# Performance work log

Measured on AMD Instinct MI355X. Metric: run time of the kernel, lower is better.

The kernel has to match this reference:

```python
import jax, jax.numpy as jnp
import numpy as np

N = 65536      # total voxels (lidar + image tokens)
D = 256        # d_model
H = 8          # nhead
DFF = 2048     # dim_feedforward
SS = 128       # set_size
SN = 512       # set_num (SN * SS == N, each partition is a permutation of all voxels)
NSHIFT = 2


def setup_inputs() -> dict:
    key = jax.random.key(0)
    ks = jax.random.split(key, 10)
    src = jax.random.normal(ks[0], (N, D), jnp.float32)
    pos_embed = jax.random.normal(ks[1], (NSHIFT, N, D), jnp.float32) * 0.02
    # each (shift, set_id) partition covers every voxel exactly once
    inds = jnp.stack([
        jnp.stack([
            jax.random.permutation(jax.random.fold_in(ks[2], s * 2 + p), N).reshape(SN, SS)
            for p in range(2)
        ])
        for s in range(NSHIFT)
    ]).astype(jnp.int32)                      # (NSHIFT, 2, SN, SS)
    masks = jax.random.uniform(ks[3], (NSHIFT, 2, SN, SS)) < 0.1
    masks = masks.at[..., 0].set(False)       # keep at least one key per set
    init = lambda k, shape: jax.random.normal(k, shape, jnp.float32) * 0.02
    return {
        'src': src, 'pos_embed': pos_embed,
        'set_voxel_inds': inds, 'set_voxel_masks': masks,
        'w_qkv': init(ks[4], (2, 3 * D, D)), 'b_qkv': jnp.zeros((2, 3 * D)),
        'w_out': init(ks[5], (2, D, D)), 'b_out': jnp.zeros((2, D)),
        'w_ff1': init(ks[6], (2, DFF, D)), 'b_ff1': jnp.zeros((2, DFF)),
        'w_ff2': init(ks[7], (2, D, DFF)), 'b_ff2': jnp.zeros((2, D)),
        'g_n1': jnp.ones((2, D)), 'b_n1': jnp.zeros((2, D)),
        'g_n2': jnp.ones((2, D)), 'b_n2': jnp.zeros((2, D)),
        'g_ln': jnp.ones((2, D)), 'b_ln': jnp.zeros((2, D)),
    }


def _ln(x, g, b):
    m = jnp.mean(x, -1, keepdims=True)
    v = jnp.mean(jnp.square(x - m), -1, keepdims=True)
    return (x - m) * jax.lax.rsqrt(v + 1e-5) * g + b


def _mha(q_in, k_in, v_in, mask, wqkv, bqkv, wo, bo):
    # q_in/k_in/v_in: (SN, SS, D); mask: (SN, SS) True = ignore key
    wq, wk, wv = jnp.split(wqkv, 3, axis=0)
    bq, bk, bv = jnp.split(bqkv, 3, axis=0)
    hd = D // H
    q = (q_in @ wq.T + bq).reshape(SN, SS, H, hd)
    k = (k_in @ wk.T + bk).reshape(SN, SS, H, hd)
    v = (v_in @ wv.T + bv).reshape(SN, SS, H, hd)
    scores = jnp.einsum('bqhd,bkhd->bhqk', q, k) / np.float32(np.sqrt(hd))
    scores = jnp.where(mask[:, None, None, :], jnp.float32(-1e9), scores)
    attn = jax.nn.softmax(scores, axis=-1)
    o = jnp.einsum('bhqk,bkhd->bqhd', attn, v).reshape(SN, SS, D)
    return o @ wo.T + bo


def reference(src, pos_embed, set_voxel_inds, set_voxel_masks,
              w_qkv, b_qkv, w_out, b_out, w_ff1, b_ff1, w_ff2, b_ff2,
              g_n1, b_n1, g_n2, b_n2, g_ln, b_ln):
    out = src
    set_id = 0  # block_id % 2 with block_id == 0
    for i in range(NSHIFT):  # two encoder layers, one per shift
        inds = set_voxel_inds[i, set_id]   # (SN, SS)
        mask = set_voxel_masks[i, set_id]  # (SN, SS)
        pos = pos_embed[i]
        identity = out
        feat = out[inds]                   # gather voxels into sets
        qk = feat + pos[inds]
        a = _mha(qk, qk, feat, mask, w_qkv[i], b_qkv[i], w_out[i], b_out[i])
        # scatter back: per voxel, take its FIRST occurrence in flattened set order
        flat = inds.reshape(-1)
        L = flat.shape[0]
        perm = jnp.full((N,), L, jnp.int32).at[flat].min(jnp.arange(L, dtype=jnp.int32))
        src2 = a.reshape(-1, D)[perm]
        x = _ln(out + src2, g_n1[i], b_n1[i])
        ff = jax.nn.relu(x @ w_ff1[i].T + b_ff1[i]) @ w_ff2[i].T + b_ff2[i]
        x = _ln(x + ff, g_n2[i], b_n2[i])
        out = _ln(x + identity, g_ln[i], b_ln[i])
    return out
```

## Files before the change

### kernel.cpp

```cpp
#include <hip/hip_runtime.h>
#include <math.h>

#define NVOX 65536
#define DM 256
#define NH 8
#define HDIM 32
#define DFFN 2048
#define SSZ 128
#define SNUM 512

#define AS1 __attribute__((address_space(1)))
#define AS3 __attribute__((address_space(3)))

typedef __attribute__((ext_vector_type(8))) __bf16 bf16x8;
typedef __attribute__((ext_vector_type(8))) unsigned short u16x8;
typedef __attribute__((ext_vector_type(4))) float f32x4;

__device__ __forceinline__ unsigned short f2bf(float f) {
    unsigned int u = __float_as_uint(f);
    u += 0x7fffu + ((u >> 16) & 1u);
    return (unsigned short)(u >> 16);
}
__device__ __forceinline__ float bf2f(unsigned short u) {
    return __uint_as_float(((unsigned int)u) << 16);
}

#define VMCNT0 asm volatile("s_waitcnt vmcnt(0)" ::: "memory")
#define VMCNT2 asm volatile("s_waitcnt vmcnt(2)" ::: "memory")
#define VMCNT4 asm volatile("s_waitcnt vmcnt(4)" ::: "memory")
#define LGKM0  asm volatile("s_waitcnt lgkmcnt(0)" ::: "memory")

__global__ __launch_bounds__(256)
void cvt_all_kernel(const float* __restrict__ a, int na,
                    const float* __restrict__ b, int nb,
                    const float* __restrict__ c, int nc,
                    const float* __restrict__ d, int nd,
                    unsigned short* __restrict__ oa, unsigned short* __restrict__ ob,
                    unsigned short* __restrict__ oc, unsigned short* __restrict__ od) {
    int i = blockIdx.x * 256 + threadIdx.x;
    int stride = gridDim.x * 256;
    int n01 = na + nb, n012 = na + nb + nc, ntot = n012 + nd;
    for (; i < ntot; i += stride) {
        if (i < na) oa[i] = f2bf(a[i]);
        else if (i < n01) ob[i - na] = f2bf(b[i - na]);
        else if (i < n012) oc[i - n01] = f2bf(c[i - n01]);
        else od[i - n012] = f2bf(d[i - n012]);
    }
}

__global__ __launch_bounds__(256)
void gather_kernel(const float* __restrict__ src, const float* __restrict__ pos,
                   const int* __restrict__ inds,
                   unsigned short* __restrict__ qk, unsigned short* __restrict__ feat) {
    int j = blockIdx.x * 4 + (threadIdx.x >> 6);
    int lane = threadIdx.x & 63;
    int v = inds[j];
    float4 a = ((const float4*)(src + (size_t)v * DM))[lane];
    float4 p = ((const float4*)(pos + (size_t)v * DM))[lane];
    ushort4 qo, fo;
    qo.x = f2bf(a.x + p.x); qo.y = f2bf(a.y + p.y);
    qo.z = f2bf(a.z + p.z); qo.w = f2bf(a.w + p.w);
    fo.x = f2bf(a.x); fo.y = f2bf(a.y); fo.z = f2bf(a.z); fo.w = f2bf(a.w);
    ((ushort4*)(qk   + (size_t)j * DM))[lane] = qo;
    ((ushort4*)(feat + (size_t)j * DM))[lane] = fo;
}

__global__ __launch_bounds__(512)
void qkv_mfma256(const unsigned short* __restrict__ Aqk, const unsigned short* __restrict__ Af,
                 const unsigned short* __restrict__ Wqkv, const float* __restrict__ bqkv,
                 unsigned short* __restrict__ Cqk, unsigned short* __restrict__ Vout) {
    __shared__ alignas(16) char smem[69632];
    unsigned short* As = (unsigned short*)smem;
    unsigned short* Bs = (unsigned short*)(smem + 32768);
    float* ebuf = (float*)smem;
    const int ES = 264;
    const int K = 256;

    int tid = threadIdx.x;
    int wave = tid >> 6, lane = tid & 63;
    int wm = wave >> 2;
    int wn = wave & 3;

    unsigned lin = blockIdx.x + blockIdx.y * gridDim.x;
    unsigned nwg = gridDim.x * gridDim.y;
    unsigned swz = lin;
    if ((nwg & 7u) == 0u) { unsigned cpx = nwg >> 3; swz = (lin & 7u) * cpx + (lin >> 3); }
    int bx = (int)(swz / gridDim.y);
    int by = (int)(swz % gridDim.y);
    int mBase = bx * 256;

    const unsigned short* A = (by < 2) ? Aqk : Af;
    int wrow0 = (by < 2) ? by * 256 : 512;
    int ncol0 = (by < 2) ? by * 256 : 0;
    int Ncols = (by < 2) ? 512 : 256;
    unsigned short* Co = (by < 2) ? Cqk : Vout;
    const float* bias = bqkv + wrow0;

    int rr = lane & 15;
    int kq = (lane >> 4) * 8;
    int rbase = (lane >> 4) * 4;

    f32x4 acc[8][4];
    const f32x4 zero = {0.f, 0.f, 0.f, 0.f};
#pragma unroll
    for (int m = 0; m < 8; m++)
#pragma unroll
        for (int n = 0; n < 4; n++) acc[m][n] = zero;

    const unsigned short* gA0 = A + (size_t)(mBase + (wave * 2 + 0) * 16 + rr) * K + kq;
    const unsigned short* gA1 = A + (size_t)(mBase + (wave * 2 + 1) * 16 + rr) * K + kq;
    const unsigned short* gB0 = Wqkv + (size_t)(wrow0 + (wave * 2 + 0) * 16 + rr) * K + kq;
    const unsigned short* gB1 = Wqkv + (size_t)(wrow0 + (wave * 2 + 1) * 16 + rr) * K + kq;

    auto stage = [&](int b, int kt) {
        int ko = kt * 32;
        __builtin_amdgcn_global_load_lds((const AS1 void*)(gA0 + ko),
            (AS3 void*)(As + b * 8192 + (wave * 2 + 0) * 512), 16, 0, 0);
        __builtin_amdgcn_global_load_lds((const AS1 void*)(gA1 + ko),
            (AS3 void*)(As + b * 8192 + (wave * 2 + 1) * 512), 16, 0, 0);
        __builtin_amdgcn_global_load_lds((const AS1 void*)(gB0 + ko),
            (AS3 void*)(Bs + b * 8192 + (wave * 2 + 0) * 512), 16, 0, 0);
        __builtin_amdgcn_global_load_lds((const AS1 void*)(gB1 + ko),
            (AS3 void*)(Bs + b * 8192 + (wave * 2 + 1) * 512), 16, 0, 0);
    };

    stage(0, 0);
    for (int t = 0; t < 8; ++t) {
        int p = t & 1;
        if (t + 1 < 8) { stage(p ^ 1, t + 1); VMCNT4; }
        else { VMCNT0; }
        __builtin_amdgcn_s_barrier();
        __builtin_amdgcn_sched_barrier(0);

        bf16x8 af[8], bf[4];
#pragma unroll
        for (int m = 0; m < 8; m++)
            af[m] = *(const bf16x8*)(As + p * 8192 + (wm * 8 + m) * 512 + lane * 8);
#pragma unroll
        for (int n = 0; n < 4; n++)
            bf[n] = *(const bf16x8*)(Bs + p * 8192 + (wn * 4 + n) * 512 + lane * 8);
#pragma unroll
        for (int m = 0; m < 8; m++)
#pragma unroll
            for (int n = 0; n < 4; n++)
                acc[m][n] = __builtin_amdgcn_mfma_f32_16x16x32_bf16(af[m], bf[n], acc[m][n], 0, 0, 0);

        __builtin_amdgcn_sched_barrier(0);
        __builtin_amdgcn_s_barrier();
    }

    float bn[4];
#pragma unroll
    for (int n = 0; n < 4; n++)
        bn[n] = bias[wn * 64 + n * 16 + rr];

    int erow = tid >> 3;
    int ec0  = (tid & 7) * 32;
#pragma unroll
    for (int pass = 0; pass < 4; ++pass) {
        __syncthreads();
        if (wm == (pass >> 1)) {
#pragma unroll
            for (int mm = 0; mm < 4; ++mm) {
                int m = (pass & 1) * 4 + mm;
#pragma unroll
                for (int n = 0; n < 4; ++n) {
                    int lcol = wn * 64 + n * 16 + rr;
#pragma unroll
                    for (int r = 0; r < 4; ++r)
                        ebuf[(mm * 16 + rbase + r) * ES + lcol] = acc[m][n][r] + bn[n];
                }
            }
        }
        __syncthreads();
        int grow = mBase + pass * 64 + erow;
        unsigned short* dst = Co + (size_t)grow * Ncols + ncol0 + ec0;
#pragma unroll
        for (int g = 0; g < 4; ++g) {
            u16x8 o;
#pragma unroll
            for (int j = 0; j < 8; ++j)
                o[j] = f2bf(ebuf[erow * ES + ec0 + g * 8 + j]);
            *(u16x8*)(dst + g * 8) = o;
        }
    }
}

__global__ __launch_bounds__(512)
void wo_mfma256(const unsigned short* __restrict__ A, const unsigned short* __restrict__ W,
                const float* __restrict__ bias,
                const int* __restrict__ inds, const float* __restrict__ res1,
                const float* __restrict__ g1, const float* __restrict__ b1,
                unsigned short* __restrict__ out2) {
    __shared__ alignas(16) char smem[69632];
    unsigned short* As = (unsigned short*)smem;
    unsigned short* Bs = (unsigned short*)(smem + 32768);
    float* ebuf = (float*)smem;
    const int ES = 264;
    const int K = 256;

    int tid = threadIdx.x;
    int wave = tid >> 6, lane = tid & 63;
    int wm = wave >> 2;
    int wn = wave & 3;

    unsigned lin = blockIdx.x;
    unsigned nwg = gridDim.x;
    unsigned swz = lin;
    if ((nwg & 7u) == 0u) { unsigned cpx = nwg >> 3; swz = (lin & 7u) * cpx + (lin >> 3); }
    int mBase = (int)swz * 256;

    int rr = lane & 15;
    int kq = (lane >> 4) * 8;
    int rbase = (lane >> 4) * 4;

    f32x4 acc[8][4];
    const f32x4 zero = {0.f, 0.f, 0.f, 0.f};
#pragma unroll
    for (int m = 0; m < 8; m++)
#pragma unroll
        for (int n = 0; n < 4; n++) acc[m][n] = zero;

    const unsigned short* gA0 = A + (size_t)(mBase + (wave * 2 + 0) * 16 + rr) * K + kq;
    const unsigned short* gA1 = A + (size_t)(mBase + (wave * 2 + 1) * 16 + rr) * K + kq;
    const unsigned short* gB0 = W + (size_t)((wave * 2 + 0) * 16 + rr) * K + kq;
    const unsigned short* gB1 = W + (size_t)((wave * 2 + 1) * 16 + rr) * K + kq;

    auto stage = [&](int b, int kt) {
        int ko = kt * 32;
        __builtin_amdgcn_global_load_lds((const AS1 void*)(gA0 + ko),
            (AS3 void*)(As + b * 8192 + (wave * 2 + 0) * 512), 16, 0, 0);
        __builtin_amdgcn_global_load_lds((const AS1 void*)(gA1 + ko),
            (AS3 void*)(As + b * 8192 + (wave * 2 + 1) * 512), 16, 0, 0);
        __builtin_amdgcn_global_load_lds((const AS1 void*)(gB0 + ko),
            (AS3 void*)(Bs + b * 8192 + (wave * 2 + 0) * 512), 16, 0, 0);
        __builtin_amdgcn_global_load_lds((const AS1 void*)(gB1 + ko),
            (AS3 void*)(Bs + b * 8192 + (wave * 2 + 1) * 512), 16, 0, 0);
    };

    stage(0, 0);
    for (int t = 0; t < 8; ++t) {
        int p = t & 1;
        if (t + 1 < 8) { stage(p ^ 1, t + 1); VMCNT4; }
        else { VMCNT0; }
        __builtin_amdgcn_s_barrier();
        __builtin_amdgcn_sched_barrier(0);

        bf16x8 af[8], bf[4];
#pragma unroll
        for (int m = 0; m < 8; m++)
            af[m] = *(const bf16x8*)(As + p * 8192 + (wm * 8 + m) * 512 + lane * 8);
#pragma unroll
        for (int n = 0; n < 4; n++)
            bf[n] = *(const bf16x8*)(Bs + p * 8192 + (wn * 4 + n) * 512 + lane * 8);
#pragma unroll
        for (int m = 0; m < 8; m++)
#pragma unroll
            for (int n = 0; n < 4; n++)
                acc[m][n] = __builtin_amdgcn_mfma_f32_16x16x32_bf16(af[m], bf[n], acc[m][n], 0, 0, 0);

        __builtin_amdgcn_sched_barrier(0);
        __builtin_amdgcn_s_barrier();
    }

    float bn[4];
#pragma unroll
    for (int n = 0; n < 4; n++)
        bn[n] = bias[wn * 64 + n * 16 + rr];

    int erow = tid >> 3;
    int ec0  = (tid & 7) * 32;
#pragma unroll
    for (int pass = 0; pass < 4; ++pass) {
        __syncthreads();
        if (wm == (pass >> 1)) {
#pragma unroll
            for (int mm = 0; mm < 4; ++mm) {
                int m = (pass & 1) * 4 + mm;
#pragma unroll
                for (int n = 0; n < 4; ++n) {
                    int lcol = wn * 64 + n * 16 + rr;
#pragma unroll
                    for (int r = 0; r < 4; ++r)
                        ebuf[(mm * 16 + rbase + r) * ES + lcol] = acc[m][n][r] + bn[n];
                }
            }
        }
        __syncthreads();
        int grow = mBase + pass * 64 + erow;
        int v = inds[grow];
        const float* pr = res1 + (size_t)v * 256;
        f32x4 tv[8];
        float s = 0.f, s2 = 0.f;
#pragma unroll
        for (int g = 0; g < 8; ++g) {
            float4 e = *(float4*)(ebuf + erow * ES + ec0 + g * 4);
            float4 p = *(const float4*)(pr + ec0 + g * 4);
            f32x4 t = {e.x + p.x, e.y + p.y, e.z + p.z, e.w + p.w};
            tv[g] = t;
            s += t[0] + t[1] + t[2] + t[3];
            s2 += t[0]*t[0] + t[1]*t[1] + t[2]*t[2] + t[3]*t[3];
        }
#pragma unroll
        for (int off = 1; off < 8; off <<= 1) { s += __shfl_xor(s, off); s2 += __shfl_xor(s2, off); }
        float mean = s * (1.f/256.f);
        float var = fmaf(-mean, mean, s2 * (1.f/256.f));
        float rs = rsqrtf(var + 1e-5f);
        unsigned short* xb = out2 + (size_t)v * 256 + ec0;
#pragma unroll
        for (int g = 0; g < 4; ++g) {
            u16x8 o;
#pragma unroll
            for (int j = 0; j < 8; ++j) {
                int idx = g * 8 + j;
                float gg = g1[ec0 + idx];
                float bb = b1[ec0 + idx];
                o[j] = f2bf(fmaf((tv[idx >> 2][idx & 3] - mean) * rs, gg, bb));
            }
            *(u16x8*)(xb + g * 8) = o;
        }
    }
}

__global__ __launch_bounds__(512, 2)
void ffn_fused(const unsigned short* __restrict__ X,
               const unsigned short* __restrict__ W1,
               const unsigned short* __restrict__ W2,
               const float* __restrict__ b1g,
               const float* __restrict__ b2g,
               const float* __restrict__ prev,
               const float* __restrict__ lnG1, const float* __restrict__ lnB1,
               const float* __restrict__ lnG2, const float* __restrict__ lnB2,
               float* __restrict__ out) {
    __shared__ alignas(16) char smem[163840];
    unsigned short* Xs   = (unsigned short*)smem;
    unsigned short* Wbuf = (unsigned short*)(smem + 65536);
    char*           HsB  = smem + 98304;
    float*          ebuf = (float*)smem;
    const int ES = 264;

    int tid = threadIdx.x;
    int wave = tid >> 6, lane = tid & 63;
    int wm = wave >> 2;
    int wn = wave & 3;
    int mBase = blockIdx.x * 128;
    int rr = lane & 15;
    int kq = (lane >> 4) * 8;
    int rbase = (lane >> 4) * 4;

    auto gll = [&](const unsigned short* g, unsigned short* l) {
        __builtin_amdgcn_global_load_lds((const AS1 void*)g, (AS3 void*)l, 16, 0, 0);
    };

#pragma unroll
    for (int u = 0; u < 8; ++u)
        gll(X + (size_t)(mBase + wave * 16 + rr) * 256 + u * 32 + kq,
            Xs + (wave * 8 + u) * 512);

    auto stage_slice = [&](int s) {
        int c = s >> 4, half = (s >> 3) & 1, kt = s & 7;
        unsigned short* wb = Wbuf + (s & 1) * 8192;
        if (half == 0) {
            gll(W1 + (size_t)(c * 256 + (wave * 2 + 0) * 16 + rr) * 256 + kt * 32 + kq,
                wb + (wave * 2 + 0) * 512);
            gll(W1 + (size_t)(c * 256 + (wave * 2 + 1) * 16 + rr) * 256 + kt * 32 + kq,
                wb + (wave * 2 + 1) * 512);
        } else {
            gll(W2 + (size_t)((wave * 2 + 0) * 16 + rr) * 2048 + c * 256 + kt * 32 + kq,
                wb + (wave * 2 + 0) * 512);
            gll(W2 + (size_t)((wave * 2 + 1) * 16 + rr) * 2048 + c * 256 + kt * 32 + kq,
                wb + (wave * 2 + 1) * 512);
        }
    };

    f32x4 yacc[4][4];
    const f32x4 zero = {0.f, 0.f, 0.f, 0.f};
#pragma unroll
    for (int m = 0; m < 4; m++)
#pragma unroll
        for (int n = 0; n < 4; n++) yacc[m][n] = zero;

    stage_slice(0);
    __syncthreads();

    for (int c = 0; c < 8; ++c) {
        f32x4 hacc[4][4];
#pragma unroll
        for (int m = 0; m < 4; m++)
#pragma unroll
            for (int n = 0; n < 4; n++) hacc[m][n] = zero;

#pragma unroll
        for (int kt = 0; kt < 8; ++kt) {
            int s = c * 16 + kt;
            stage_slice(s + 1);
            VMCNT2;
            __builtin_amdgcn_s_barrier();
            __builtin_amdgcn_sched_barrier(0);

            bf16x8 af[4], bf[4];
#pragma unroll
            for (int m = 0; m < 4; m++)
                af[m] = *(const bf16x8*)(Xs + ((wm * 4 + m) * 8 + kt) * 512 + lane * 8);
#pragma unroll
            for (int n = 0; n < 4; n++)
                bf[n] = *(const bf16x8*)(Wbuf + (s & 1) * 8192 + (wn * 4 + n) * 512 + lane * 8);
#pragma unroll
            for (int m = 0; m < 4; m++)
#pragma unroll
                for (int n = 0; n < 4; n++)
                    hacc[m][n] = __builtin_amdgcn_mfma_f32_16x16x32_bf16(af[m], bf[n], hacc[m][n], 0, 0, 0);

            __builtin_amdgcn_sched_barrier(0);
            __builtin_amdgcn_s_barrier();
        }

        {
            float b1v[4];
#pragma unroll
            for (int n = 0; n < 4; n++)
                b1v[n] = b1g[c * 256 + wn * 64 + n * 16 + rr];
#pragma unroll
            for (int m = 0; m < 4; m++)
#pragma unroll
                for (int n = 0; n < 4; n++)
#pragma unroll
                    for (int r = 0; r < 4; r++) {
                        float v = fmaxf(hacc[m][n][r] + b1v[n], 0.f);
                        int row = wm * 64 + m * 16 + rbase + r;
                        int col = wn * 64 + n * 16 + rr;
                        unsigned byte = (unsigned)(row * 512 + col * 2) ^ ((row & 7) << 4);
                        *(unsigned short*)(HsB + byte) = f2bf(v);
                    }
            LGKM0;
            __builtin_amdgcn_s_barrier();
        }

#pragma unroll
        for (int kt = 0; kt < 8; ++kt) {
            int s = c * 16 + 8 + kt;
            if (s + 1 < 128) { stage_slice(s + 1); VMCNT2; }
            else { VMCNT0; }
            __builtin_amdgcn_s_barrier();
            __builtin_amdgcn_sched_barrier(0);

            bf16x8 af[4], bf[4];
#pragma unroll
            for (int m = 0; m < 4; m++) {
                int row = wm * 64 + m * 16 + rr;
                unsigned byte = (unsigned)(row * 512 + kt * 64 + (lane >> 4) * 16) ^ ((rr & 7) << 4);
                af[m] = *(const bf16x8*)(HsB + byte);
            }
#pragma unroll
            for (int n = 0; n < 4; n++)
                bf[n] = *(const bf16x8*)(Wbuf + (s & 1) * 8192 + (wn * 4 + n) * 512 + lane * 8);
#pragma unroll
            for (int m = 0; m < 4; m++)
#pragma unroll
                for (int n = 0; n < 4; n++)
                    yacc[m][n] = __builtin_amdgcn_mfma_f32_16x16x32_bf16(af[m], bf[n], yacc[m][n], 0, 0, 0);

            __builtin_amdgcn_sched_barrier(0);
            __builtin_amdgcn_s_barrier();
        }
    }

    float b2v[4];
#pragma unroll
    for (int n = 0; n < 4; n++)
        b2v[n] = b2g[wn * 64 + n * 16 + rr];

    int erow = tid >> 5;
    int ec0  = (tid & 31) * 8;
#pragma unroll
    for (int p = 0; p < 8; ++p) {
        __syncthreads();
        if (wm == (p >> 2)) {
            const int m = p & 3;
#pragma unroll
            for (int n = 0; n < 4; ++n) {
                int lcol = wn * 64 + n * 16 + rr;
#pragma unroll
                for (int r = 0; r < 4; ++r)
                    ebuf[(rbase + r) * ES + lcol] = yacc[m][n][r] + b2v[n];
            }
        }
        __syncthreads();
        int grow = mBase + p * 16 + erow;

        float tv[8];
        float s1 = 0.f, s2 = 0.f;
        const unsigned short* xr = X + (size_t)grow * 256 + ec0;
        u16x8 xv = *(const u16x8*)xr;
#pragma unroll
        for (int j = 0; j < 8; ++j) {
            float t = ebuf[erow * ES + ec0 + j] + bf2f(xv[j]);
            tv[j] = t; s1 += t; s2 += t * t;
        }
#pragma unroll
        for (int off = 1; off < 32; off <<= 1) { s1 += __shfl_xor(s1, off); s2 += __shfl_xor(s2, off); }
        float mean = s1 * (1.f/256.f);
        float var = fmaf(-mean, mean, s2 * (1.f/256.f));
        float rs = rsqrtf(var + 1e-5f);

        const float* pr = prev + (size_t)grow * 256 + ec0;
        float s3 = 0.f, s4 = 0.f;
#pragma unroll
        for (int j = 0; j < 8; ++j) {
            float u = fmaf((tv[j] - mean) * rs, lnG1[ec0 + j], lnB1[ec0 + j]) + pr[j];
            tv[j] = u; s3 += u; s4 += u * u;
        }
#pragma unroll
        for (int off = 1; off < 32; off <<= 1) { s3 += __shfl_xor(s3, off); s4 += __shfl_xor(s4, off); }
        float mean2 = s3 * (1.f/256.f);
        float var2 = fmaf(-mean2, mean2, s4 * (1.f/256.f));
        float rs2 = rsqrtf(var2 + 1e-5f);

        float* od = out + (size_t)grow * 256 + ec0;
#pragma unroll
        for (int g = 0; g < 2; ++g) {
            float4 o;
            o.x = fmaf((tv[g*4+0] - mean2) * rs2, lnG2[ec0 + g*4+0], lnB2[ec0 + g*4+0]);
            o.y = fmaf((tv[g*4+1] - mean2) * rs2, lnG2[ec0 + g*4+1], lnB2[ec0 + g*4+1]);
            o.z = fmaf((tv[g*4+2] - mean2) * rs2, lnG2[ec0 + g*4+2], lnB2[ec0 + g*4+2]);
            o.w = fmaf((tv[g*4+3] - mean2) * rs2, lnG2[ec0 + g*4+3], lnB2[ec0 + g*4+3]);
            *(float4*)(od + g * 4) = o;
        }
    }
}

__global__ __launch_bounds__(256)
void attn_mfma_kernel(const unsigned short* __restrict__ QK,
                      const unsigned short* __restrict__ V,
                      const unsigned char* __restrict__ mask,
                      unsigned short* __restrict__ ao) {
    int s = blockIdx.x, h = blockIdx.y;
    int tid = threadIdx.x;
    int wq = tid >> 6;
    int lane = tid & 63;

    __shared__ alignas(16) unsigned short Ks[128 * 40];
    __shared__ alignas(16) unsigned short Vt[32 * 136];
    __shared__ alignas(16) unsigned short Plds[4 * 4096];
    __shared__ unsigned char msk[SSZ];

#pragma unroll
    for (int it = 0; it < 2; it++) {
        int idx = tid + it * 256;
        int key = idx >> 2, dimoff = (idx & 3) * 8;
        bf16x8 kv = *(const bf16x8*)(QK + (size_t)(s * SSZ + key) * 512 + 256 + h * HDIM + dimoff);
        *(bf16x8*)(Ks + key * 40 + dimoff) = kv;
        u16x8 vv = *(const u16x8*)(V + (size_t)(s * SSZ + key) * DM + h * HDIM + dimoff);
#pragma unroll
        for (int j = 0; j < 8; j++) Vt[(dimoff + j) * 136 + key] = vv[j];
    }
    if (tid < SSZ) msk[tid] = mask[s * SSZ + tid];
    __syncthreads();

    int rr = lane & 15;
    int kq = (lane >> 4) * 8;
    const f32x4 zero = {0.f, 0.f, 0.f, 0.f};

    bf16x8 qa[2];
#pragma unroll
    for (int mt = 0; mt < 2; mt++)
        qa[mt] = *(const bf16x8*)(QK + (size_t)(s * SSZ + wq * 32 + mt * 16 + rr) * 512 + h * HDIM + kq);

    f32x4 S[2][8];
    __builtin_amdgcn_s_setprio(1);
#pragma unroll
    for (int nt = 0; nt < 8; nt++) {
        bf16x8 kb = *(const bf16x8*)(Ks + (nt * 16 + rr) * 40 + kq);
#pragma unroll
        for (int mt = 0; mt < 2; mt++)
            S[mt][nt] = __builtin_amdgcn_mfma_f32_16x16x32_bf16(qa[mt], kb, zero, 0, 0, 0);
    }
    __builtin_amdgcn_s_setprio(0);

    const float SCALE = 0.17677669529663687f;
    f32x4 rm[2];
#pragma unroll
    for (int mt = 0; mt < 2; mt++) { rm[mt].x = rm[mt].y = rm[mt].z = rm[mt].w = -1e30f; }
#pragma unroll
    for (int nt = 0; nt < 8; nt++) {
        bool mv = msk[nt * 16 + rr] != 0;
#pragma unroll
        for (int mt = 0; mt < 2; mt++) {
#pragma unroll
            for (int r = 0; r < 4; r++) {
                float v = mv ? -1e30f : S[mt][nt][r] * SCALE;
                S[mt][nt][r] = v;
                rm[mt][r] = fmaxf(rm[mt][r], v);
            }
        }
    }
#pragma unroll
    for (int off = 1; off < 16; off <<= 1) {
#pragma unroll
        for (int mt = 0; mt < 2; mt++)
#pragma unroll
            for (int r = 0; r < 4; r++)
                rm[mt][r] = fmaxf(rm[mt][r], __shfl_xor(rm[mt][r], off));
    }

    f32x4 rs[2];
#pragma unroll
    for (int mt = 0; mt < 2; mt++) { rs[mt] = zero; }
#pragma unroll
    for (int nt = 0; nt < 8; nt++)
#pragma unroll
        for (int mt = 0; mt < 2; mt++)
#pragma unroll
            for (int r = 0; r < 4; r++) {
                float p = __expf(S[mt][nt][r] - rm[mt][r]);
                S[mt][nt][r] = p;
                rs[mt][r] += p;
            }
#pragma unroll
    for (int off = 1; off < 16; off <<= 1) {
#pragma unroll
        for (int mt = 0; mt < 2; mt++)
#pragma unroll
            for (int r = 0; r < 4; r++)
                rs[mt][r] += __shfl_xor(rs[mt][r], off);
    }

    char* Pbase = (char*)Plds + wq * 8192;
#pragma unroll
    for (int nt = 0; nt < 8; nt++)
#pragma unroll
        for (int mt = 0; mt < 2; mt++)
#pragma unroll
            for (int r = 0; r < 4; r++) {
                int prow = mt * 16 + (lane >> 4) * 4 + r;
                int col  = nt * 16 + rr;
                unsigned addr = (unsigned)(prow * 256 + col * 2) ^ ((prow & 7) << 4);
                *(unsigned short*)(Pbase + addr) = f2bf(S[mt][nt][r]);
            }
    __syncthreads();

    f32x4 O[2][2];
#pragma unroll
    for (int mt = 0; mt < 2; mt++)
#pragma unroll
        for (int nd = 0; nd < 2; nd++) O[mt][nd] = zero;
    __builtin_amdgcn_s_setprio(1);
#pragma unroll
    for (int kc = 0; kc < 4; kc++) {
        bf16x8 pa[2];
#pragma unroll
        for (int mt = 0; mt < 2; mt++) {
            int prow = mt * 16 + rr;
            unsigned addr = (unsigned)(prow * 256 + (kc * 32 + kq) * 2) ^ ((prow & 7) << 4);
            pa[mt] = *(const bf16x8*)(Pbase + addr);
        }
#pragma unroll
        for (int nd = 0; nd < 2; nd++) {
            bf16x8 vb = *(const bf16x8*)(Vt + (nd * 16 + rr) * 136 + kc * 32 + kq);
#pragma unroll
            for (int mt = 0; mt < 2; mt++)
                O[mt][nd] = __builtin_amdgcn_mfma_f32_16x16x32_bf16(pa[mt], vb, O[mt][nd], 0, 0, 0);
        }
    }
    __builtin_amdgcn_s_setprio(0);

#pragma unroll
    for (int mt = 0; mt < 2; mt++) {
#pragma unroll
        for (int nd = 0; nd < 2; nd++) {
#pragma unroll
            for (int r = 0; r < 4; r++) {
                int row = s * SSZ + wq * 32 + mt * 16 + (lane >> 4) * 4 + r;
                int col = h * HDIM + nd * 16 + rr;
                ao[(size_t)row * DM + col] = f2bf(O[mt][nd][r] / rs[mt][r]);
            }
        }
    }
}

extern "C" void kernel_launch(void* const* d_in, const int* in_sizes, int n_in,
                              void* d_out, int out_size, void* d_ws, size_t ws_size,
                              hipStream_t stream) {
    const float* src       = (const float*)d_in[0];
    const float* pos_embed = (const float*)d_in[1];
    const int*   inds_all  = (const int*)d_in[2];
    const unsigned char* masks_all = (const unsigned char*)d_in[3];
    const float* w_qkv = (const float*)d_in[4];
    const float* b_qkv = (const float*)d_in[5];
    const float* w_out = (const float*)d_in[6];
    const float* b_out = (const float*)d_in[7];
    const float* w_ff1 = (const float*)d_in[8];
    const float* b_ff1 = (const float*)d_in[9];
    const float* w_ff2 = (const float*)d_in[10];
    const float* b_ff2 = (const float*)d_in[11];
    const float* g_n1 = (const float*)d_in[12];
    const float* b_n1 = (const float*)d_in[13];
    const float* g_n2 = (const float*)d_in[14];
    const float* b_n2 = (const float*)d_in[15];
    const float* g_ln = (const float*)d_in[16];
    const float* b_ln = (const float*)d_in[17];
    float* out = (float*)d_out;

    const size_t NVF = (size_t)NVOX * DM;
    unsigned short* A = (unsigned short*)d_ws;
    unsigned short* B = A + NVF;
    unsigned short* C = B + NVF;
    unsigned short* D = C + 2 * NVF;
    unsigned short* wts = D + NVF;
    const size_t SZ_QKV = (size_t)2 * 3 * DM * DM;
    const size_t SZ_WO  = (size_t)2 * DM * DM;
    const size_t SZ_FF1 = (size_t)2 * DFFN * DM;
    const size_t SZ_FF2 = (size_t)2 * DM * DFFN;
    unsigned short* wqkv_bf = wts;
    unsigned short* wo_bf   = wqkv_bf + SZ_QKV;
    unsigned short* wff1_bf = wo_bf + SZ_WO;
    unsigned short* wff2_bf = wff1_bf + SZ_FF1;

    cvt_all_kernel<<<1024, 256, 0, stream>>>(
        w_qkv, (int)SZ_QKV, w_out, (int)SZ_WO, w_ff1, (int)SZ_FF1, w_ff2, (int)SZ_FF2,
        wqkv_bf, wo_bf, wff1_bf, wff2_bf);

    for (int i = 0; i < 2; i++) {
        const float* prev = (i == 0) ? src : out;
        const int* inds = inds_all + (size_t)i * 2 * SNUM * SSZ;
        const unsigned char* mask = masks_all + (size_t)i * 2 * SNUM * SSZ;
        const float* pos  = pos_embed + (size_t)i * NVF;
        const unsigned short* wqkv = wqkv_bf + (size_t)i * 3 * DM * DM;
        const unsigned short* wo   = wo_bf + (size_t)i * DM * DM;
        const unsigned short* wff1 = wff1_bf + (size_t)i * DFFN * DM;
        const unsigned short* wff2 = wff2_bf + (size_t)i * DM * DFFN;
        const float* bqkv = b_qkv + (size_t)i * 3 * DM;
        const float* bo   = b_out + (size_t)i * DM;
        const float* bff1 = b_ff1 + (size_t)i * DFFN;
        const float* bff2 = b_ff2 + (size_t)i * DM;

        gather_kernel<<<NVOX / 4, 256, 0, stream>>>(prev, pos, inds, A, B);

        qkv_mfma256<<<dim3(NVOX / 256, 3), 512, 0, stream>>>(
            A, B, wqkv, bqkv, C, D);

        attn_mfma_kernel<<<dim3(SNUM, NH), 256, 0, stream>>>(C, D, mask, A);

        wo_mfma256<<<dim3(NVOX / 256), 512, 0, stream>>>(
            A, wo, bo, inds, prev, g_n1 + i * DM, b_n1 + i * DM, B);

        ffn_fused<<<dim3(NVOX / 128), 512, 0, stream>>>(
            B, wff1, wff2, bff1, bff2, prev,
            g_n2 + i * DM, b_n2 + i * DM, g_ln + i * DM, b_ln + i * DM, out);
    }
}
```

Measured before the change: 950.4 us.

## Load FFN weight fragments directly into registers with double-buffering, dropping LDS staging

The fused FFN kernel stops staging W1/W2 slices through shared memory with global_load_lds and per-k-step barriers. Each wave now loads its own weight fragments straight from global memory into two register buffers, prefetched two steps ahead, and the inner-loop barriers are removed. Shared memory falls to 128KB and launch bounds go to one block per CU, trading occupancy for fewer syncs and less LDS traffic. The catch is that each wave-column re-fetches weights redundantly from global/L2, and the loads use uncoalesced 16-byte row strides.

```diff
diff --git a/kernel.cpp b/kernel.cpp
--- a/kernel.cpp
+++ b/kernel.cpp
@@ -26,7 +26,6 @@
 }
 
 #define VMCNT0 asm volatile("s_waitcnt vmcnt(0)" ::: "memory")
-#define VMCNT2 asm volatile("s_waitcnt vmcnt(2)" ::: "memory")
 #define VMCNT4 asm volatile("s_waitcnt vmcnt(4)" ::: "memory")
 #define LGKM0  asm volatile("s_waitcnt lgkmcnt(0)" ::: "memory")
 
@@ -322,7 +321,7 @@
     }
 }
 
-__global__ __launch_bounds__(512, 2)
+__global__ __launch_bounds__(512, 1)
 void ffn_fused(const unsigned short* __restrict__ X,
                const unsigned short* __restrict__ W1,
                const unsigned short* __restrict__ W2,
@@ -332,10 +331,9 @@
                const float* __restrict__ lnG1, const float* __restrict__ lnB1,
                const float* __restrict__ lnG2, const float* __restrict__ lnB2,
                float* __restrict__ out) {
-    __shared__ alignas(16) char smem[163840];
-    unsigned short* Xs   = (unsigned short*)smem;
-    unsigned short* Wbuf = (unsigned short*)(smem + 65536);
-    char*           HsB  = smem + 98304;
+    __shared__ alignas(16) char smem[131072];
+    unsigned short* Xs = (unsigned short*)smem;
+    char*           HsB = smem + 65536;
     float*          ebuf = (float*)smem;
     const int ES = 264;
 
@@ -348,28 +346,22 @@
     int kq = (lane >> 4) * 8;
     int rbase = (lane >> 4) * 4;
 
-    auto gll = [&](const unsigned short* g, unsigned short* l) {
-        __builtin_amdgcn_global_load_lds((const AS1 void*)g, (AS3 void*)l, 16, 0, 0);
-    };
-
 #pragma unroll
     for (int u = 0; u < 8; ++u)
-        gll(X + (size_t)(mBase + wave * 16 + rr) * 256 + u * 32 + kq,
-            Xs + (wave * 8 + u) * 512);
-
-    auto stage_slice = [&](int s) {
+        __builtin_amdgcn_global_load_lds(
+            (const AS1 void*)(X + (size_t)(mBase + wave * 16 + rr) * 256 + u * 32 + kq),
+            (AS3 void*)(Xs + (wave * 8 + u) * 512), 16, 0, 0);
+
+    auto loadW = [&](int s, bf16x8* dst) {
         int c = s >> 4, half = (s >> 3) & 1, kt = s & 7;
-        unsigned short* wb = Wbuf + (s & 1) * 8192;
         if (half == 0) {
-            gll(W1 + (size_t)(c * 256 + (wave * 2 + 0) * 16 + rr) * 256 + kt * 32 + kq,
-                wb + (wave * 2 + 0) * 512);
-            gll(W1 + (size_t)(c * 256 + (wave * 2 + 1) * 16 + rr) * 256 + kt * 32 + kq,
-                wb + (wave * 2 + 1) * 512);
+#pragma unroll
+            for (int n = 0; n < 4; n++)
+                dst[n] = *(const bf16x8*)(W1 + (size_t)(c * 256 + wn * 64 + n * 16 + rr) * 256 + kt * 32 + kq);
         } else {
-            gll(W2 + (size_t)((wave * 2 + 0) * 16 + rr) * 2048 + c * 256 + kt * 32 + kq,
-                wb + (wave * 2 + 0) * 512);
-            gll(W2 + (size_t)((wave * 2 + 1) * 16 + rr) * 2048 + c * 256 + kt * 32 + kq,
-                wb + (wave * 2 + 1) * 512);
+#pragma unroll
+            for (int n = 0; n < 4; n++)
+                dst[n] = *(const bf16x8*)(W2 + (size_t)(wn * 64 + n * 16 + rr) * 2048 + c * 256 + kt * 32 + kq);
         }
     };
 
@@ -380,10 +372,13 @@
 #pragma unroll
         for (int n = 0; n < 4; n++) yacc[m][n] = zero;
 
-    stage_slice(0);
+    bf16x8 wA[4], wB[4];
+    loadW(0, wA);
+    loadW(1, wB);
     __syncthreads();
 
     for (int c = 0; c < 8; ++c) {
+        int s0 = c * 16;
         f32x4 hacc[4][4];
 #pragma unroll
         for (int m = 0; m < 4; m++)
@@ -391,30 +386,30 @@
             for (int n = 0; n < 4; n++) hacc[m][n] = zero;
 
 #pragma unroll
-        for (int kt = 0; kt < 8; ++kt) {
-            int s = c * 16 + kt;
-            stage_slice(s + 1);
-            VMCNT2;
-            __builtin_amdgcn_s_barrier();
-            __builtin_amdgcn_sched_barrier(0);
-
-            bf16x8 af[4], bf[4];
+        for (int kt = 0; kt < 8; kt += 2) {
+            bf16x8 af[4];
 #pragma unroll
             for (int m = 0; m < 4; m++)
                 af[m] = *(const bf16x8*)(Xs + ((wm * 4 + m) * 8 + kt) * 512 + lane * 8);
 #pragma unroll
-            for (int n = 0; n < 4; n++)
-                bf[n] = *(const bf16x8*)(Wbuf + (s & 1) * 8192 + (wn * 4 + n) * 512 + lane * 8);
-#pragma unroll
             for (int m = 0; m < 4; m++)
 #pragma unroll
                 for (int n = 0; n < 4; n++)
-                    hacc[m][n] = __builtin_amdgcn_mfma_f32_16x16x32_bf16(af[m], bf[n], hacc[m][n], 0, 0, 0);
-
-            __builtin_amdgcn_sched_barrier(0);
-            __builtin_amdgcn_s_barrier();
-        }
-
+                    hacc[m][n] = __builtin_amdgcn_mfma_f32_16x16x32_bf16(af[m], wA[n], hacc[m][n], 0, 0, 0);
+            loadW(s0 + kt + 2, wA);
+
+#pragma unroll
+            for (int m = 0; m < 4; m++)
+                af[m] = *(const bf16x8*)(Xs + ((wm * 4 + m) * 8 + kt + 1) * 512 + lane * 8);
+#pragma unroll
+            for (int m = 0; m < 4; m++)
+#pragma unroll
+                for (int n = 0; n < 4; n++)
+                    hacc[m][n] = __builtin_amdgcn_mfma_f32_16x16x32_bf16(af[m], wB[n], hacc[m][n], 0, 0, 0);
+            loadW(s0 + kt + 3, wB);
+        }
+
+        __builtin_amdgcn_s_barrier();
         {
             float b1v[4];
 #pragma unroll
@@ -437,14 +432,8 @@
         }
 
 #pragma unroll
-        for (int kt = 0; kt < 8; ++kt) {
-            int s = c * 16 + 8 + kt;
-            if (s + 1 < 128) { stage_slice(s + 1); VMCNT2; }
-            else { VMCNT0; }
-            __builtin_amdgcn_s_barrier();
-            __builtin_amdgcn_sched_barrier(0);
-
-            bf16x8 af[4], bf[4];
+        for (int kt = 0; kt < 8; kt += 2) {
+            bf16x8 af[4];
 #pragma unroll
             for (int m = 0; m < 4; m++) {
                 int row = wm * 64 + m * 16 + rr;
@@ -452,16 +441,24 @@
                 af[m] = *(const bf16x8*)(HsB + byte);
             }
 #pragma unroll
-            for (int n = 0; n < 4; n++)
-                bf[n] = *(const bf16x8*)(Wbuf + (s & 1) * 8192 + (wn * 4 + n) * 512 + lane * 8);
-#pragma unroll
             for (int m = 0; m < 4; m++)
 #pragma unroll
                 for (int n = 0; n < 4; n++)
-                    yacc[m][n] = __builtin_amdgcn_mfma_f32_16x16x32_bf16(af[m], bf[n], yacc[m][n], 0, 0, 0);
-
-            __builtin_amdgcn_sched_barrier(0);
-            __builtin_amdgcn_s_barrier();
+                    yacc[m][n] = __builtin_amdgcn_mfma_f32_16x16x32_bf16(af[m], wA[n], yacc[m][n], 0, 0, 0);
+            if (s0 + kt + 10 < 128) loadW(s0 + kt + 10, wA);
+
+#pragma unroll
+            for (int m = 0; m < 4; m++) {
+                int row = wm * 64 + m * 16 + rr;
+                unsigned byte = (unsigned)(row * 512 + (kt + 1) * 64 + (lane >> 4) * 16) ^ ((rr & 7) << 4);
+                af[m] = *(const bf16x8*)(HsB + byte);
+            }
+#pragma unroll
+            for (int m = 0; m < 4; m++)
+#pragma unroll
+                for (int n = 0; n < 4; n++)
+                    yacc[m][n] = __builtin_amdgcn_mfma_f32_16x16x32_bf16(af[m], wB[n], yacc[m][n], 0, 0, 0);
+            if (s0 + kt + 11 < 128) loadW(s0 + kt + 11, wB);
         }
     }
 
```

Measured after the change: 1.122 ms. 1.18x slower.
